# Kernel tuning notes

Measured on AMD Instinct MI355X. Metric: run time of the kernel, lower is better.

Reference implementation:

```python
import jax, jax.numpy as jnp
import numpy as np
import math
from jax import lax

L, E, H, F = 4, 1024, 16, 4096
B, S = 8, 512
VV, VR = 40, 30
DIST_V = 200
PAD_ID = 0


def setup_inputs() -> dict:
    key = jax.random.key(0)
    ks = iter(jax.random.split(key, 32))
    w = lambda *sh: jax.random.normal(next(ks), sh, jnp.float32) * 0.02
    inp = {
        'val_emb': w(VV, E),
        'ring_emb': w(VR, E),
        'dist_emb': w(DIST_V, H),
        'Wqkv': w(L, 3 * E, E), 'bqkv': jnp.zeros((L, 3 * E), jnp.float32),
        'Wo': w(L, E, E), 'bo': jnp.zeros((L, E), jnp.float32),
        'ln1_s': jnp.ones((L, E), jnp.float32), 'ln1_b': jnp.zeros((L, E), jnp.float32),
        'W1': w(L, F, E), 'b1': jnp.zeros((L, F), jnp.float32),
        'W2': w(L, E, F), 'b2': jnp.zeros((L, E), jnp.float32),
        'ln2_s': jnp.ones((L, E), jnp.float32), 'ln2_b': jnp.zeros((L, E), jnp.float32),
        'lnf_s': jnp.ones((E,), jnp.float32), 'lnf_b': jnp.zeros((E,), jnp.float32),
        'gen_W': w(VV * VR, E), 'gen_b': jnp.zeros((VV * VR,), jnp.float32),
    }
    val = jax.random.randint(next(ks), (B, S), 0, VV)
    val = val.at[:, 0].set(1)  # ensure first key is never <pad> (id 0)
    inp['val_sequences'] = val
    inp['ring_sequences'] = jax.random.randint(next(ks), (B, S), 0, VR)
    inp['distance_squares'] = jax.random.randint(next(ks), (B, S, S), 0, DIST_V)
    return inp


def _ln(x, s, b):
    m = x.mean(-1, keepdims=True)
    v = ((x - m) ** 2).mean(-1, keepdims=True)
    return (x - m) / jnp.sqrt(v + 1e-5) * s + b


def _forward(val_emb, ring_emb, dist_emb, Wqkv, bqkv, Wo, bo, ln1_s, ln1_b,
             W1, b1, W2, b2, ln2_s, ln2_b, lnf_s, lnf_b, gen_W, gen_b,
             val_sequences, ring_sequences, distance_squares):
    Bv, Sv = val_sequences.shape
    dh = E // H
    scale = 1.0 / math.sqrt(dh)
    # token embeddings, each scaled by sqrt(emb_size)
    x = (val_emb[val_sequences] + ring_emb[ring_sequences]) * math.sqrt(E)  # [B,S,E]
    # distance bias [B,S,S,H] -> [B,H,S,S], causal fill with -inf, key padding -inf
    bias = jnp.transpose(dist_emb[distance_squares], (0, 3, 1, 2))
    causal = jnp.tril(jnp.ones((Sv, Sv), bool))
    mask = jnp.where(causal[None, None], bias, -jnp.inf)
    pad = (val_sequences == PAD_ID)  # [B,S]
    mask = jnp.where(pad[:, None, None, :], -jnp.inf, mask)

    def step(h, p):
        wqkv, bq, wo, bo_, l1s, l1b, w1, b1_, w2, b2_, l2s, l2b = p
        qkv = h @ wqkv.T + bq  # [B,S,3E]
        q, k, v = jnp.split(qkv, 3, axis=-1)
        q = q.reshape(Bv, Sv, H, dh).transpose(0, 2, 1, 3)
        k = k.reshape(Bv, Sv, H, dh).transpose(0, 2, 1, 3)
        v = v.reshape(Bv, Sv, H, dh).transpose(0, 2, 1, 3)
        scores = jnp.einsum('bhqd,bhkd->bhqk', q, k) * scale + mask
        a = jax.nn.softmax(scores, axis=-1)
        ctx = jnp.einsum('bhqk,bhkd->bhqd', a, v)
        ctx = ctx.transpose(0, 2, 1, 3).reshape(Bv, Sv, E)
        h = _ln(h + ctx @ wo.T + bo_, l1s, l1b)  # post-norm
        ff = jax.nn.gelu(h @ w1.T + b1_, approximate=False) @ w2.T + b2_
        h = _ln(h + ff, l2s, l2b)
        return h, None

    layer_params = (Wqkv, bqkv, Wo, bo, ln1_s, ln1_b, W1, b1, W2, b2, ln2_s, ln2_b)
    x, _ = lax.scan(step, x, layer_params)
    x = _ln(x, lnf_s, lnf_b)
    return x @ gen_W.T + gen_b  # [B,S,VV*VR]


def reference(val_emb, ring_emb, dist_emb, Wqkv, bqkv, Wo, bo, ln1_s, ln1_b,
              W1, b1, W2, b2, ln2_s, ln2_b, lnf_s, lnf_b, gen_W, gen_b,
              val_sequences, ring_sequences, distance_squares):
    return _forward(val_emb, ring_emb, dist_emb, Wqkv, bqkv, Wo, bo, ln1_s, ln1_b,
                    W1, b1, W2, b2, ln2_s, ln2_b, lnf_s, lnf_b, gen_W, gen_b,
                    val_sequences, ring_sequences, distance_squares)
```

## Files before the change

### kernel.cpp

```cpp
#include <hip/hip_runtime.h>
#include <hip/hip_bf16.h>

typedef __attribute__((ext_vector_type(8))) short bf16x8;
typedef __attribute__((ext_vector_type(4))) float f32x4;
typedef unsigned short u16;
typedef __attribute__((ext_vector_type(4))) unsigned short u16x4;

#define L_ 4
#define E_ 1024
#define H_ 16
#define F_ 4096
#define B_ 8
#define S_ 512
#define T_ 4096
#define GEN_N 1200
#define GEN_PAD 1280
#define D8S 528

#define AS1 __attribute__((address_space(1)))
#define AS3 __attribute__((address_space(3)))

static __device__ __forceinline__ u16 f2bf(float f) {
  unsigned u = __float_as_uint(f);
  unsigned r = (u + 0x7fffu + ((u >> 16) & 1u)) >> 16;
  return (u16)r;
}

static __device__ __forceinline__ unsigned cvt_pk_bf16(float lo, float hi) {
  unsigned r;
  asm("v_cvt_pk_bf16_f32 %0, %1, %2" : "=v"(r) : "v"(lo), "v"(hi));
  return r;
}

static __device__ __forceinline__ float fast_gelu(float v) {
  float y = 0.7978845608f * (v + 0.044715f * v * v * v);
  y = fminf(fmaxf(y, -9.f), 9.f);
  float e2 = __expf(2.f * y);
  float th = (e2 - 1.f) / (e2 + 1.f);
  return 0.5f * v * (1.f + th);
}

__global__ __launch_bounds__(256) void cvt_bf16(const float* __restrict__ src,
                                                u16* __restrict__ dst, int n) {
  int i = (blockIdx.x * 256 + threadIdx.x) * 4;
  if (i >= n) return;
  float4 v = *reinterpret_cast<const float4*>(src + i);
  u16x4 o = {f2bf(v.x), f2bf(v.y), f2bf(v.z), f2bf(v.w)};
  *reinterpret_cast<u16x4*>(dst + i) = o;
}

__global__ __launch_bounds__(256) void cvt4_k(const float* __restrict__ s0,
                                              const float* __restrict__ s1,
                                              const float* __restrict__ s2,
                                              const float* __restrict__ s3,
                                              u16* __restrict__ d0, u16* __restrict__ d1,
                                              u16* __restrict__ d2, u16* __restrict__ d3) {
  int q = blockIdx.x * 256 + threadIdx.x;
  const float* s;
  u16* d;
  int i;
  if (q < 786432) { s = s0; d = d0; i = q; }
  else if (q < 786432 + 262144) { s = s1; d = d1; i = q - 786432; }
  else if (q < 786432 + 262144 + 1048576) { s = s2; d = d2; i = q - (786432 + 262144); }
  else { s = s3; d = d3; i = q - (786432 + 262144 + 1048576); }
  i *= 4;
  float4 v = *reinterpret_cast<const float4*>(s + i);
  u16x4 o = {f2bf(v.x), f2bf(v.y), f2bf(v.z), f2bf(v.w)};
  *reinterpret_cast<u16x4*>(d + i) = o;
}

__global__ __launch_bounds__(256) void d8pre_k(const int* __restrict__ dist,
                                               const int* __restrict__ vseq,
                                               unsigned char* __restrict__ d8g) {
  int idx = blockIdx.x * 256 + threadIdx.x;
  int k4 = idx & 127;
  int b = idx >> 16;
  int4 dv = *reinterpret_cast<const int4*>(dist + (size_t)idx * 4);
  int4 vv = *reinterpret_cast<const int4*>(vseq + b * S_ + k4 * 4);
  uchar4 o;
  o.x = (vv.x == 0) ? (unsigned char)200 : (unsigned char)dv.x;
  o.y = (vv.y == 0) ? (unsigned char)200 : (unsigned char)dv.y;
  o.z = (vv.z == 0) ? (unsigned char)200 : (unsigned char)dv.z;
  o.w = (vv.w == 0) ? (unsigned char)200 : (unsigned char)dv.w;
  *reinterpret_cast<uchar4*>(d8g + (size_t)idx * 4) = o;
}

__global__ __launch_bounds__(256) void embed_k(const float* __restrict__ val_emb,
                                               const float* __restrict__ ring_emb,
                                               const int* __restrict__ vseq,
                                               const int* __restrict__ rseq,
                                               float* __restrict__ h, u16* __restrict__ xbf) {
  int tok = blockIdx.x;
  int e = threadIdx.x * 4;
  int v = vseq[tok], r = rseq[tok];
  float4 a = *reinterpret_cast<const float4*>(val_emb + v * E_ + e);
  float4 b = *reinterpret_cast<const float4*>(ring_emb + r * E_ + e);
  float4 o;
  o.x = (a.x + b.x) * 32.f; o.y = (a.y + b.y) * 32.f;
  o.z = (a.z + b.z) * 32.f; o.w = (a.w + b.w) * 32.f;
  *reinterpret_cast<float4*>(h + (size_t)tok * E_ + e) = o;
  u16x4 ob = {f2bf(o.x), f2bf(o.y), f2bf(o.z), f2bf(o.w)};
  *reinterpret_cast<u16x4*>(xbf + (size_t)tok * E_ + e) = ob;
}

__global__ __launch_bounds__(256) void ln_k(const float* hin, const float* add0,
                                            const float* add1, const float* cbias,
                                            const float* g, const float* bta,
                                            float* hout, u16* xout) {
  int tok = blockIdx.x * 4 + (threadIdx.x >> 6);
  int lane = threadIdx.x & 63;
  const float* hp = hin + (size_t)tok * E_;
  float4 v[4];
  #pragma unroll
  for (int p = 0; p < 4; ++p) {
    int e = p * 256 + lane * 4;
    v[p] = *reinterpret_cast<const float4*>(hp + e);
    if (add0) {
      float4 a0 = *reinterpret_cast<const float4*>(add0 + (size_t)tok * E_ + e);
      float4 a1 = *reinterpret_cast<const float4*>(add1 + (size_t)tok * E_ + e);
      float4 cb = *reinterpret_cast<const float4*>(cbias + e);
      v[p].x += a0.x + a1.x + cb.x; v[p].y += a0.y + a1.y + cb.y;
      v[p].z += a0.z + a1.z + cb.z; v[p].w += a0.w + a1.w + cb.w;
    }
  }
  float s = 0.f, q = 0.f;
  #pragma unroll
  for (int p = 0; p < 4; ++p) {
    s += v[p].x + v[p].y + v[p].z + v[p].w;
    q += v[p].x * v[p].x + v[p].y * v[p].y + v[p].z * v[p].z + v[p].w * v[p].w;
  }
  #pragma unroll
  for (int off = 1; off < 64; off <<= 1) {
    s += __shfl_xor(s, off, 64);
    q += __shfl_xor(q, off, 64);
  }
  float mean = s * (1.f / E_);
  float var = q * (1.f / E_) - mean * mean;
  float inv = rsqrtf(var + 1e-5f);
  #pragma unroll
  for (int p = 0; p < 4; ++p) {
    int e = p * 256 + lane * 4;
    float4 gg = *reinterpret_cast<const float4*>(g + e);
    float4 bb = *reinterpret_cast<const float4*>(bta + e);
    float4 o;
    o.x = (v[p].x - mean) * inv * gg.x + bb.x;
    o.y = (v[p].y - mean) * inv * gg.y + bb.y;
    o.z = (v[p].z - mean) * inv * gg.z + bb.z;
    o.w = (v[p].w - mean) * inv * gg.w + bb.w;
    if (hout) *reinterpret_cast<float4*>(hout + (size_t)tok * E_ + e) = o;
    u16x4 ob = {f2bf(o.x), f2bf(o.y), f2bf(o.z), f2bf(o.w)};
    *reinterpret_cast<u16x4*>(xout + (size_t)tok * E_ + e) = ob;
  }
}

template <int EPI>
__global__ __launch_bounds__(256, 2) void gemm_small(const u16* __restrict__ A,
                                                     const u16* __restrict__ W,
                                                     const float* __restrict__ bias,
                                                     void* __restrict__ Cp,
                                                     u16* __restrict__ Vt,
                                                     int M, int N, int K, int tilesN) {
  __shared__ __align__(16) char lds[49152];
  int tid = threadIdx.x;
  int wid = tid >> 6, l = tid & 63;
  int wm = wid >> 1, wn = wid & 1;
  int lr = l & 15, lk = l >> 4;
  int nwg = gridDim.x, bid = blockIdx.x;
  int swz = ((nwg & 7) == 0) ? ((bid & 7) * (nwg >> 3) + (bid >> 3)) : bid;
  int tm = swz / tilesN, tn = swz % tilesN;
  int row0 = tm * 128, col0 = tn * 256;

  int srow = tid >> 2;
  int sch = ((tid & 3) ^ ((srow >> 1) & 3)) * 8;
  const u16* gA = A + (size_t)(row0 + srow) * K + sch;
  const u16* gB = W + (size_t)(col0 + srow) * K + sch;
  int wslot = wid * 1024;

  auto stage = [&](int buf, int kt) {
    size_t ko = (size_t)kt * 32;
    int base = buf * 24576;
    #pragma unroll
    for (int i = 0; i < 2; ++i)
      __builtin_amdgcn_global_load_lds((const AS1 void*)(gA + (size_t)i * 64 * K + ko),
                                       (AS3 void*)(lds + base + i * 4096 + wslot), 16, 0, 0);
    #pragma unroll
    for (int i = 0; i < 4; ++i)
      __builtin_amdgcn_global_load_lds((const AS1 void*)(gB + (size_t)i * 64 * K + ko),
                                       (AS3 void*)(lds + base + 8192 + i * 4096 + wslot), 16, 0, 0);
  };

  int ck = (lk ^ ((lr >> 1) & 3)) * 16;
  f32x4 acc[4][8];
  f32x4 z = {0.f, 0.f, 0.f, 0.f};
  #pragma unroll
  for (int m = 0; m < 4; ++m)
    #pragma unroll
    for (int n = 0; n < 8; ++n) acc[m][n] = z;

  auto compute = [&](int buf) {
    int base = buf * 24576;
    bf16x8 bfr[8];
    #pragma unroll
    for (int n = 0; n < 8; ++n)
      bfr[n] = *reinterpret_cast<const bf16x8*>(lds + base + 8192 + (wn * 128 + n * 16 + lr) * 64 + ck);
    #pragma unroll
    for (int m = 0; m < 4; ++m) {
      bf16x8 af = *reinterpret_cast<const bf16x8*>(lds + base + (wm * 64 + m * 16 + lr) * 64 + ck);
      #pragma unroll
      for (int n = 0; n < 8; ++n)
        acc[m][n] = __builtin_amdgcn_mfma_f32_16x16x32_bf16(af, bfr[n], acc[m][n], 0, 0, 0);
    }
  };

  int nt = K >> 5;
  stage(0, 0);
  int cur = 0;
  for (int t = 0; t < nt; ++t) {
    if (t + 1 < nt) {
      stage(cur ^ 1, t + 1);
      asm volatile("s_waitcnt vmcnt(6)" ::: "memory");
    } else {
      asm volatile("s_waitcnt vmcnt(0)" ::: "memory");
    }
    __builtin_amdgcn_s_barrier();
    asm volatile("" ::: "memory");
    compute(cur);
    asm volatile("" ::: "memory");
    __builtin_amdgcn_s_barrier();
    cur ^= 1;
  }

  #pragma unroll
  for (int n = 0; n < 8; ++n) {
    int col = col0 + wn * 128 + n * 16 + lr;
    float bv = bias[col];
    #pragma unroll
    for (int m = 0; m < 4; ++m) {
      int rbase = row0 + wm * 64 + m * 16 + lk * 4;
      #pragma unroll
      for (int r2 = 0; r2 < 4; ++r2) {
        float v = acc[m][n][r2] + bv;
        if (EPI == 1) v = fast_gelu(v);
        int row = rbase + r2;
        u16 bw = f2bf(v);
        ((u16*)Cp)[(size_t)row * N + col] = bw;
        if (EPI == 0 && Vt != nullptr && col >= 2 * E_) {
          int dg = col - 2 * E_;
          int hh = dg >> 6, dd = dg & 63;
          int bb = row >> 9, ss = row & 511;
          Vt[((size_t)((bb * 16 + hh) * 64 + dd) << 9) + ss] = bw;
        }
      }
    }
  }
}

template <int EPI, int NW, int SPLITK>
__global__ __launch_bounds__(512, 2) void gemm_big(const u16* __restrict__ A,
                                                   const u16* __restrict__ W,
                                                   const float* __restrict__ bias,
                                                   void* __restrict__ Cp,
                                                   int M, int N, int K, int tilesN) {
  constexpr int BN = 64 * NW;
  __shared__ __align__(16) u16 As[2][256 * 64];
  __shared__ __align__(16) u16 Bs[2][BN * 64];
  int tid = threadIdx.x;
  int wid = tid >> 6, ln = tid & 63;
  int wm = wid >> 2, wn = wid & 3;
  int lr = ln & 15, lk = ln >> 4;
  int nwg = gridDim.x;
  int bid = blockIdx.x;
  int swz = ((nwg & 7) == 0) ? ((bid & 7) * (nwg >> 3) + (bid >> 3)) : bid;
  int sp = 0, tile = swz;
  if (SPLITK > 1) { sp = swz & (SPLITK - 1); tile = swz / SPLITK; }
  int tm = tile / tilesN, tn = tile % tilesN;
  int row0 = tm * 256, col0 = tn * BN;
  int Ks = K / SPLITK;
  int kbase = sp * Ks;

  int srow = tid >> 3;
  int schunk = ((tid & 7) ^ (srow & 7)) * 8;
  const u16* gA = A + (size_t)(row0 + srow) * K + kbase + schunk;
  const u16* gB = W + (size_t)(col0 + srow) * K + kbase + schunk;
  size_t ldsBase = (size_t)((wid << 3) * 64) * 2;

  auto stage = [&](int buf, int kt) {
    size_t ko = (size_t)kt * 64;
    #pragma unroll
    for (int i = 0; i < 4; ++i)
      __builtin_amdgcn_global_load_lds(
          (const AS1 void*)(gA + (size_t)i * 64 * K + ko),
          (AS3 void*)((char*)&As[buf][0] + ldsBase + (size_t)i * 64 * 128), 16, 0, 0);
    #pragma unroll
    for (int i = 0; i < NW; ++i)
      __builtin_amdgcn_global_load_lds(
          (const AS1 void*)(gB + (size_t)i * 64 * K + ko),
          (AS3 void*)((char*)&Bs[buf][0] + ldsBase + (size_t)i * 64 * 128), 16, 0, 0);
  };

  f32x4 acc[8][NW];
  f32x4 z = {0.f, 0.f, 0.f, 0.f};
  #pragma unroll
  for (int m = 0; m < 8; ++m)
    #pragma unroll
    for (int n = 0; n < NW; ++n) acc[m][n] = z;

  auto compute = [&](int buf) {
    #pragma unroll
    for (int s = 0; s < 2; ++s) {
      int ch = ((s * 4 + lk) ^ (lr & 7)) * 8;
      bf16x8 bfr[NW];
      #pragma unroll
      for (int n = 0; n < NW; ++n)
        bfr[n] = *reinterpret_cast<const bf16x8*>(&Bs[buf][(wn * (16 * NW) + n * 16 + lr) * 64 + ch]);
      #pragma unroll
      for (int m = 0; m < 8; ++m) {
        bf16x8 af = *reinterpret_cast<const bf16x8*>(&As[buf][(wm * 128 + m * 16 + lr) * 64 + ch]);
        #pragma unroll
        for (int n = 0; n < NW; ++n)
          acc[m][n] = __builtin_amdgcn_mfma_f32_16x16x32_bf16(af, bfr[n], acc[m][n], 0, 0, 0);
      }
    }
  };

  int nt = Ks >> 6;
  stage(0, 0);
  int cur = 0;
  for (int t = 0; t < nt; ++t) {
    if (t + 1 < nt) {
      stage(cur ^ 1, t + 1);
      if constexpr (NW == 2) asm volatile("s_waitcnt vmcnt(6)" ::: "memory");
      else if constexpr (NW == 3) asm volatile("s_waitcnt vmcnt(7)" ::: "memory");
      else asm volatile("s_waitcnt vmcnt(8)" ::: "memory");
    } else {
      asm volatile("s_waitcnt vmcnt(0)" ::: "memory");
    }
    __builtin_amdgcn_s_barrier();
    asm volatile("" ::: "memory");
    compute(cur);
    asm volatile("" ::: "memory");
    __builtin_amdgcn_s_barrier();
    cur ^= 1;
  }

  #pragma unroll
  for (int n = 0; n < NW; ++n) {
    int col = col0 + wn * (16 * NW) + n * 16 + lr;
    if (col >= N) continue;
    float bv = (EPI == 2) ? 0.f : bias[col];
    #pragma unroll
    for (int m = 0; m < 8; ++m) {
      int rbase = row0 + wm * 128 + m * 16 + lk * 4;
      #pragma unroll
      for (int r2 = 0; r2 < 4; ++r2) {
        float v = acc[m][n][r2] + bv;
        int row = rbase + r2;
        if (EPI == 2)
          ((float*)Cp)[(size_t)sp * M * N + (size_t)row * N + col] = v;
        else
          ((float*)Cp)[(size_t)row * N + col] = v;
      }
    }
  }
}

__global__ __launch_bounds__(256, 4) void attn_fused_k(const u16* __restrict__ qkv,
                                                       const unsigned char* __restrict__ d8g,
                                                       const float* __restrict__ dist_emb,
                                                       const u16* __restrict__ Vt,
                                                       u16* __restrict__ ctx) {
  int blk = blockIdx.x;
  int bh = blk & 127;
  int qt = blk >> 7;
  int b = bh >> 4, h = bh & 15;
  int tid = threadIdx.x, wv = tid >> 6, l = tid & 63;
  int lr = l & 15, lk = l >> 4;

  __shared__ float de[208];
  __shared__ __align__(16) unsigned char d8[64 * D8S];

  int ncol = (qt + 1) * 64;
  for (int i = tid; i < 208; i += 256)
    de[i] = (i < 200) ? dist_emb[i * H_ + h] : -1e30f;
  {
    int r = tid >> 2;
    const unsigned char* srow = d8g + ((size_t)(b * S_ + qt * 64 + r) << 9);
    int nc16 = ncol >> 4;
    for (int c = (tid & 3); c < nc16; c += 4) {
      int4 v = *reinterpret_cast<const int4*>(srow + c * 16);
      *reinterpret_cast<int4*>(&d8[r * D8S + c * 16]) = v;
    }
  }
  __syncthreads();

  int q0 = qt * 64 + wv * 16;
  int nv = 4 * qt + wv + 1;
  int qglob = q0 + lr;
  int qloc = wv * 16 + lr;

  bf16x8 aq0 = *reinterpret_cast<const bf16x8*>(
      qkv + (size_t)(b * S_ + q0 + lr) * 3072 + h * 64 + lk * 8);
  bf16x8 aq1 = *reinterpret_cast<const bf16x8*>(
      qkv + (size_t)(b * S_ + q0 + lr) * 3072 + h * 64 + 32 + lk * 8);

  float sm = 0.f;
  f32x4 z = {0.f, 0.f, 0.f, 0.f};
  f32x4 acc_o[4] = {z, z, z, z};

  int sA = lr + ((2 * lk) & 3) * 16;
  int sB = lr + ((2 * lk + 1) & 3) * 16;
  int jsel = (lk >= 2);

  const u16* kBase = qkv + (size_t)(b * S_ + lr) * 3072 + E_ + h * 64 + lk * 8;
  const u16* vBase = Vt + (size_t)(bh * 64 + lr) * S_ + lk * 8;

  int ngroups = (nv + 1) >> 1;
  #pragma unroll 1
  for (int g = 0; g < ngroups; ++g) {
    f32x4 s0 = z, s1 = z;
    {
      const u16* kb = kBase + (size_t)(2 * g) * 16 * 3072;
      bf16x8 bk0 = *reinterpret_cast<const bf16x8*>(kb);
      bf16x8 bk1 = *reinterpret_cast<const bf16x8*>(kb + 32);
      s0 = __builtin_amdgcn_mfma_f32_16x16x32_bf16(bk0, aq0, s0, 0, 0, 0);
      s0 = __builtin_amdgcn_mfma_f32_16x16x32_bf16(bk1, aq1, s0, 0, 0, 0);
    }
    if (2 * g + 1 < nv) {
      const u16* kb = kBase + (size_t)(2 * g + 1) * 16 * 3072;
      bf16x8 bk0 = *reinterpret_cast<const bf16x8*>(kb);
      bf16x8 bk1 = *reinterpret_cast<const bf16x8*>(kb + 32);
      s1 = __builtin_amdgcn_mfma_f32_16x16x32_bf16(bk0, aq0, s1, 0, 0, 0);
      s1 = __builtin_amdgcn_mfma_f32_16x16x32_bf16(bk1, aq1, s1, 0, 0, 0);
    }
    float e0[4], e1[4];
    {
      unsigned dd = *reinterpret_cast<const unsigned*>(&d8[qloc * D8S + (2 * g) * 16 + lk * 4]);
      #pragma unroll
      for (int r2 = 0; r2 < 4; ++r2) {
        int kg = (2 * g) * 16 + lk * 4 + r2;
        float e = 0.f;
        if (kg <= qglob)
          e = __expf(s0[r2] * 0.125f + de[(dd >> (8 * r2)) & 255]);
        e0[r2] = e; sm += e;
      }
    }
    {
      unsigned dd = *reinterpret_cast<const unsigned*>(&d8[qloc * D8S + (2 * g + 1) * 16 + lk * 4]);
      #pragma unroll
      for (int r2 = 0; r2 < 4; ++r2) {
        int kg = (2 * g + 1) * 16 + lk * 4 + r2;
        float e = 0.f;
        if (2 * g + 1 < nv && kg <= qglob)
          e = __expf(s1[r2] * 0.125f + de[(dd >> (8 * r2)) & 255]);
        e1[r2] = e; sm += e;
      }
    }
    unsigned t0p0 = cvt_pk_bf16(e0[0], e0[1]);
    unsigned t0p1 = cvt_pk_bf16(e0[2], e0[3]);
    unsigned t1p0 = cvt_pk_bf16(e1[0], e1[1]);
    unsigned t1p1 = cvt_pk_bf16(e1[2], e1[3]);
    unsigned a00 = __shfl((int)t0p0, sA, 64), a10 = __shfl((int)t1p0, sA, 64);
    unsigned a01 = __shfl((int)t0p1, sA, 64), a11 = __shfl((int)t1p1, sA, 64);
    unsigned b00 = __shfl((int)t0p0, sB, 64), b10 = __shfl((int)t1p0, sB, 64);
    unsigned b01 = __shfl((int)t0p1, sB, 64), b11 = __shfl((int)t1p1, sB, 64);
    unsigned w0 = jsel ? a10 : a00;
    unsigned w1 = jsel ? a11 : a01;
    unsigned w2 = jsel ? b10 : b00;
    unsigned w3 = jsel ? b11 : b01;
    bf16x8 pfrag;
    {
      unsigned pw[4] = {w0, w1, w2, w3};
      pfrag = *reinterpret_cast<bf16x8*>(pw);
    }
    const u16* vb = vBase + g * 32;
    acc_o[0] = __builtin_amdgcn_mfma_f32_16x16x32_bf16(
        *reinterpret_cast<const bf16x8*>(vb), pfrag, acc_o[0], 0, 0, 0);
    acc_o[1] = __builtin_amdgcn_mfma_f32_16x16x32_bf16(
        *reinterpret_cast<const bf16x8*>(vb + 16 * S_), pfrag, acc_o[1], 0, 0, 0);
    acc_o[2] = __builtin_amdgcn_mfma_f32_16x16x32_bf16(
        *reinterpret_cast<const bf16x8*>(vb + 32 * S_), pfrag, acc_o[2], 0, 0, 0);
    acc_o[3] = __builtin_amdgcn_mfma_f32_16x16x32_bf16(
        *reinterpret_cast<const bf16x8*>(vb + 48 * S_), pfrag, acc_o[3], 0, 0, 0);
  }

  sm += __shfl_xor(sm, 16, 64);
  sm += __shfl_xor(sm, 32, 64);
  float il = 1.f / sm;

  #pragma unroll
  for (int n4 = 0; n4 < 4; ++n4) {
    u16x4 o;
    o.x = f2bf(acc_o[n4][0] * il);
    o.y = f2bf(acc_o[n4][1] * il);
    o.z = f2bf(acc_o[n4][2] * il);
    o.w = f2bf(acc_o[n4][3] * il);
    *reinterpret_cast<u16x4*>(ctx + (size_t)(b * S_ + qglob) * E_ + h * 64 + n4 * 16 + lk * 4) = o;
  }
}

extern "C" void kernel_launch(void* const* d_in, const int* in_sizes, int n_in,
                              void* d_out, int out_size, void* d_ws, size_t ws_size,
                              hipStream_t stream) {
  const float* val_emb = (const float*)d_in[0];
  const float* ring_emb = (const float*)d_in[1];
  const float* dist_emb = (const float*)d_in[2];
  const float* Wqkv = (const float*)d_in[3];
  const float* bqkv = (const float*)d_in[4];
  const float* Wo = (const float*)d_in[5];
  const float* bo = (const float*)d_in[6];
  const float* ln1_s = (const float*)d_in[7];
  const float* ln1_b = (const float*)d_in[8];
  const float* W1 = (const float*)d_in[9];
  const float* b1 = (const float*)d_in[10];
  const float* W2 = (const float*)d_in[11];
  const float* b2 = (const float*)d_in[12];
  const float* ln2_s = (const float*)d_in[13];
  const float* ln2_b = (const float*)d_in[14];
  const float* lnf_s = (const float*)d_in[15];
  const float* lnf_b = (const float*)d_in[16];
  const float* gen_W = (const float*)d_in[17];
  const float* gen_b = (const float*)d_in[18];
  const int* vseq = (const int*)d_in[19];
  const int* rseq = (const int*)d_in[20];
  const int* dist = (const int*)d_in[21];

  char* ws = (char*)d_ws;
  size_t off = 0;
  auto alloc = [&](size_t nbytes) {
    char* p = ws + off;
    off += (nbytes + 255) & ~(size_t)255;
    return p;
  };
  u16* gw_bf = (u16*)alloc((size_t)GEN_PAD * E_ * 2);
  u16* wqkv_l = (u16*)alloc((size_t)3 * E_ * E_ * 2);
  u16* wo_l = (u16*)alloc((size_t)E_ * E_ * 2);
  u16* w1_l = (u16*)alloc((size_t)F_ * E_ * 2);
  u16* w2_l = (u16*)alloc((size_t)E_ * F_ * 2);
  float* h = (float*)alloc((size_t)T_ * E_ * 4);
  u16* x_bf = (u16*)alloc((size_t)T_ * E_ * 2);
  u16* qkv_bf = (u16*)alloc((size_t)T_ * 3 * E_ * 2);
  u16* ctx_bf = (u16*)alloc((size_t)T_ * E_ * 2);
  u16* vt_bf = (u16*)alloc((size_t)B_ * H_ * 64 * S_ * 2);
  unsigned char* d8g = (unsigned char*)alloc((size_t)B_ * S_ * S_);
  u16* p_bf = (u16*)alloc((size_t)B_ * H_ * S_ * S_ * 2);
  u16* ff_bf = p_bf;
  float* psum = (float*)(p_bf + (size_t)T_ * F_);
  (void)ws_size; (void)in_sizes; (void)n_in; (void)out_size; (void)rseq;

  cvt_bf16<<<dim3((GEN_N * E_ / 4 + 255) / 256), dim3(256), 0, stream>>>(gen_W, gw_bf,
                                                                         GEN_N * E_);
  d8pre_k<<<dim3(B_ * S_ * S_ / 4 / 256), dim3(256), 0, stream>>>(dist, vseq, d8g);
  embed_k<<<dim3(T_), dim3(256), 0, stream>>>(val_emb, ring_emb, vseq, rseq, h, x_bf);

  for (int l = 0; l < L_; ++l) {
    cvt4_k<<<dim3(12288), dim3(256), 0, stream>>>(
        Wqkv + (size_t)l * 3 * E_ * E_, Wo + (size_t)l * E_ * E_,
        W1 + (size_t)l * F_ * E_, W2 + (size_t)l * E_ * F_,
        wqkv_l, wo_l, w1_l, w2_l);

    gemm_small<0><<<dim3(384), dim3(256), 0, stream>>>(
        x_bf, wqkv_l, bqkv + (size_t)l * 3 * E_, qkv_bf, vt_bf, T_, 3 * E_, E_, 12);
    attn_fused_k<<<dim3(B_ * H_ * 8), dim3(256), 0, stream>>>(qkv_bf, d8g, dist_emb,
                                                              vt_bf, ctx_bf);
    gemm_big<2, 2, 2><<<dim3(256), dim3(512), 0, stream>>>(
        ctx_bf, wo_l, nullptr, psum, T_, E_, E_, 8);
    ln_k<<<dim3(T_ / 4), dim3(256), 0, stream>>>(h, psum, psum + (size_t)T_ * E_,
                                                 bo + (size_t)l * E_,
                                                 ln1_s + (size_t)l * E_, ln1_b + (size_t)l * E_,
                                                 h, x_bf);
    gemm_small<1><<<dim3(512), dim3(256), 0, stream>>>(
        x_bf, w1_l, b1 + (size_t)l * F_, ff_bf, nullptr, T_, F_, E_, 16);
    gemm_big<2, 2, 2><<<dim3(256), dim3(512), 0, stream>>>(
        ff_bf, w2_l, nullptr, psum, T_, E_, F_, 8);
    ln_k<<<dim3(T_ / 4), dim3(256), 0, stream>>>(h, psum, psum + (size_t)T_ * E_,
                                                 b2 + (size_t)l * E_,
                                                 ln2_s + (size_t)l * E_, ln2_b + (size_t)l * E_,
                                                 h, x_bf);
  }
  ln_k<<<dim3(T_ / 4), dim3(256), 0, stream>>>(h, nullptr, nullptr, nullptr, lnf_s, lnf_b,
                                               nullptr, x_bf);
  gemm_big<3, 2, 1><<<dim3(160), dim3(512), 0, stream>>>(
      x_bf, gw_bf, gen_b, (float*)d_out, T_, GEN_N, E_, 10);
}
```

Measured before the change: 1.022 ms.

## Add 256x256 ping-pong GEMM kernel for FFN and split W2 GEMM four ways

Adds a new 512-thread GEMM kernel, gemm8p. It uses 256x256 tiles, a swizzled LDS layout and eight interleaved compute phases with staged loads and priority bumps, and it replaces the W1 and W2 FFN GEMMs. The W2 GEMM now uses split-K of 4 with partials written to two buffers, one of them reusing the qkv buffer. The layernorm kernel takes two extra partial-sum inputs to reduce these. The intent is larger tile reuse and better MFMA/load overlap. The cost is higher register and LDS pressure at occupancy 1, plus extra partial traffic in the LN.

```diff
diff --git a/kernel.cpp b/kernel.cpp
--- a/kernel.cpp
+++ b/kernel.cpp
@@ -104,7 +104,8 @@
 }
 
 __global__ __launch_bounds__(256) void ln_k(const float* hin, const float* add0,
-                                            const float* add1, const float* cbias,
+                                            const float* add1, const float* add2,
+                                            const float* add3, const float* cbias,
                                             const float* g, const float* bta,
                                             float* hout, u16* xout) {
   int tok = blockIdx.x * 4 + (threadIdx.x >> 6);
@@ -121,6 +122,12 @@
       float4 cb = *reinterpret_cast<const float4*>(cbias + e);
       v[p].x += a0.x + a1.x + cb.x; v[p].y += a0.y + a1.y + cb.y;
       v[p].z += a0.z + a1.z + cb.z; v[p].w += a0.w + a1.w + cb.w;
+      if (add2) {
+        float4 a2 = *reinterpret_cast<const float4*>(add2 + (size_t)tok * E_ + e);
+        float4 a3 = *reinterpret_cast<const float4*>(add3 + (size_t)tok * E_ + e);
+        v[p].x += a2.x + a3.x; v[p].y += a2.y + a3.y;
+        v[p].z += a2.z + a3.z; v[p].w += a2.w + a3.w;
+      }
     }
   }
   float s = 0.f, q = 0.f;
@@ -150,6 +157,178 @@
     if (hout) *reinterpret_cast<float4*>(hout + (size_t)tok * E_ + e) = o;
     u16x4 ob = {f2bf(o.x), f2bf(o.y), f2bf(o.z), f2bf(o.w)};
     *reinterpret_cast<u16x4*>(xout + (size_t)tok * E_ + e) = ob;
+  }
+}
+
+template <int EPI, int SPLITK>
+__global__ __launch_bounds__(512, 1) void gemm8p(const u16* __restrict__ A,
+                                                 const u16* __restrict__ W,
+                                                 const float* __restrict__ bias,
+                                                 void* __restrict__ Cp,
+                                                 float* __restrict__ Cp2,
+                                                 int M, int N, int K, int tilesN) {
+  __shared__ __align__(16) u16 As[2][256 * 64];
+  __shared__ __align__(16) u16 Bs[2][256 * 64];
+  int tid = threadIdx.x;
+  int wid = tid >> 6, l = tid & 63;
+  int wm = wid >> 2, wn = wid & 3;
+  int lr = l & 15, lk = l >> 4;
+  int nwg = gridDim.x, bid = blockIdx.x;
+  int swz = ((nwg & 7) == 0) ? ((bid & 7) * (nwg >> 3) + (bid >> 3)) : bid;
+  int sp = 0, tile = swz;
+  if (SPLITK > 1) { sp = swz & (SPLITK - 1); tile = swz / SPLITK; }
+  int tm = tile / tilesN, tn = tile % tilesN;
+  int row0 = tm * 256, col0 = tn * 256;
+  int Ks = K / SPLITK, kbase = sp * Ks;
+
+  int srow = tid >> 3;
+  int schunk = ((tid & 7) ^ (srow & 7)) * 8;
+  const u16* gA = A + (size_t)(row0 + srow) * K + kbase + schunk;
+  const u16* gB = W + (size_t)(col0 + srow) * K + kbase + schunk;
+  size_t ldsBase = (size_t)wid * 1024;
+
+  auto stageHalf = [&](int buf, int kt, int half) {
+    size_t ko = (size_t)kt * 64;
+    if (half == 0) {
+      __builtin_amdgcn_global_load_lds((const AS1 void*)(gA + ko),
+          (AS3 void*)((char*)&As[buf][0] + ldsBase), 16, 0, 0);
+      __builtin_amdgcn_global_load_lds((const AS1 void*)(gA + (size_t)64 * K + ko),
+          (AS3 void*)((char*)&As[buf][0] + 8192 + ldsBase), 16, 0, 0);
+    } else if (half == 1) {
+      __builtin_amdgcn_global_load_lds((const AS1 void*)(gA + (size_t)128 * K + ko),
+          (AS3 void*)((char*)&As[buf][0] + 16384 + ldsBase), 16, 0, 0);
+      __builtin_amdgcn_global_load_lds((const AS1 void*)(gA + (size_t)192 * K + ko),
+          (AS3 void*)((char*)&As[buf][0] + 24576 + ldsBase), 16, 0, 0);
+    } else if (half == 2) {
+      __builtin_amdgcn_global_load_lds((const AS1 void*)(gB + ko),
+          (AS3 void*)((char*)&Bs[buf][0] + ldsBase), 16, 0, 0);
+      __builtin_amdgcn_global_load_lds((const AS1 void*)(gB + (size_t)64 * K + ko),
+          (AS3 void*)((char*)&Bs[buf][0] + 8192 + ldsBase), 16, 0, 0);
+    } else {
+      __builtin_amdgcn_global_load_lds((const AS1 void*)(gB + (size_t)128 * K + ko),
+          (AS3 void*)((char*)&Bs[buf][0] + 16384 + ldsBase), 16, 0, 0);
+      __builtin_amdgcn_global_load_lds((const AS1 void*)(gB + (size_t)192 * K + ko),
+          (AS3 void*)((char*)&Bs[buf][0] + 24576 + ldsBase), 16, 0, 0);
+    }
+  };
+
+  f32x4 acc[8][4];
+  f32x4 z = {0.f, 0.f, 0.f, 0.f};
+  #pragma unroll
+  for (int m = 0; m < 8; ++m)
+    #pragma unroll
+    for (int n = 0; n < 4; ++n) acc[m][n] = z;
+
+  bf16x8 aF[4][2], aS[4][2], bF[2][2], bS[2][2];
+
+  auto ldA4 = [&](bf16x8 (&dst)[4][2], int buf, int mBase) {
+    #pragma unroll
+    for (int m = 0; m < 4; ++m)
+      #pragma unroll
+      for (int s = 0; s < 2; ++s) {
+        int row = wm * 128 + (mBase + m) * 16 + lr;
+        int ch = ((s * 4 + lk) ^ (lr & 7)) * 8;
+        dst[m][s] = *reinterpret_cast<const bf16x8*>(&As[buf][row * 64 + ch]);
+      }
+  };
+  auto ldB2 = [&](bf16x8 (&dst)[2][2], int buf, int nBase) {
+    #pragma unroll
+    for (int n = 0; n < 2; ++n)
+      #pragma unroll
+      for (int s = 0; s < 2; ++s) {
+        int row = wn * 64 + (nBase + n) * 16 + lr;
+        int ch = ((s * 4 + lk) ^ (lr & 7)) * 8;
+        dst[n][s] = *reinterpret_cast<const bf16x8*>(&Bs[buf][row * 64 + ch]);
+      }
+  };
+
+#define PHASE_HEAD() \
+    asm volatile("" ::: "memory"); \
+    __builtin_amdgcn_s_barrier(); \
+    asm volatile("s_waitcnt lgkmcnt(0)" ::: "memory"); \
+    __builtin_amdgcn_s_setprio(1);
+#define PHASE_TAIL() \
+    __builtin_amdgcn_s_setprio(0); \
+    asm volatile("" ::: "memory"); \
+    __builtin_amdgcn_s_barrier(); \
+    asm volatile("" ::: "memory");
+#define MM_Q(AREG, BREG, MB, NB) \
+    _Pragma("unroll") \
+    for (int m = 0; m < 4; ++m) \
+      _Pragma("unroll") \
+      for (int n = 0; n < 2; ++n) \
+        _Pragma("unroll") \
+        for (int s = 0; s < 2; ++s) \
+          acc[(MB) + m][(NB) + n] = __builtin_amdgcn_mfma_f32_16x16x32_bf16( \
+              AREG[m][s], BREG[n][s], acc[(MB) + m][(NB) + n], 0, 0, 0);
+
+  int nt = Ks >> 6;
+  int nIter = nt >> 1;
+  stageHalf(0, 0, 0); stageHalf(0, 0, 1); stageHalf(0, 0, 2); stageHalf(0, 0, 3);
+  stageHalf(1, 1, 0);
+  asm volatile("s_waitcnt vmcnt(2)" ::: "memory");
+  __builtin_amdgcn_s_barrier();
+  asm volatile("" ::: "memory");
+
+  for (int i = 0; i < nIter; ++i) {
+    int a = 2 * i, b = 2 * i + 1;
+    bool notLast = (i < nIter - 1);
+    ldA4(aF, 0, 0); ldB2(bF, 0, 0);
+    stageHalf(1, b, 1);
+    PHASE_HEAD(); MM_Q(aF, bF, 0, 0); PHASE_TAIL();
+    ldB2(bS, 0, 2);
+    stageHalf(1, b, 2);
+    PHASE_HEAD(); MM_Q(aF, bS, 0, 2); PHASE_TAIL();
+    ldA4(aS, 0, 4);
+    stageHalf(1, b, 3);
+    PHASE_HEAD(); MM_Q(aS, bF, 4, 0); PHASE_TAIL();
+    if (notLast) {
+      stageHalf(0, a + 2, 0);
+      asm volatile("s_waitcnt vmcnt(2)" ::: "memory");
+    } else {
+      asm volatile("s_waitcnt vmcnt(0)" ::: "memory");
+    }
+    PHASE_HEAD(); MM_Q(aS, bS, 4, 2); PHASE_TAIL();
+    ldA4(aF, 1, 0); ldB2(bF, 1, 0);
+    if (notLast) stageHalf(0, a + 2, 1);
+    PHASE_HEAD(); MM_Q(aF, bF, 0, 0); PHASE_TAIL();
+    ldB2(bS, 1, 2);
+    if (notLast) stageHalf(0, a + 2, 2);
+    PHASE_HEAD(); MM_Q(aF, bS, 0, 2); PHASE_TAIL();
+    ldA4(aS, 1, 4);
+    if (notLast) stageHalf(0, a + 2, 3);
+    PHASE_HEAD(); MM_Q(aS, bF, 4, 0); PHASE_TAIL();
+    if (notLast) {
+      stageHalf(1, b + 2, 0);
+      asm volatile("s_waitcnt vmcnt(2)" ::: "memory");
+    }
+    PHASE_HEAD(); MM_Q(aS, bS, 4, 2); PHASE_TAIL();
+  }
+#undef PHASE_HEAD
+#undef PHASE_TAIL
+#undef MM_Q
+
+  #pragma unroll
+  for (int n = 0; n < 4; ++n) {
+    int col = col0 + wn * 64 + n * 16 + lr;
+    if (col >= N) continue;
+    float bv = (EPI == 2) ? 0.f : bias[col];
+    #pragma unroll
+    for (int m = 0; m < 8; ++m) {
+      int rbase = row0 + wm * 128 + m * 16 + lk * 4;
+      #pragma unroll
+      for (int r2 = 0; r2 < 4; ++r2) {
+        float v = acc[m][n][r2] + bv;
+        if (EPI == 1) v = fast_gelu(v);
+        int row = rbase + r2;
+        if (EPI == 2) {
+          float* dst = (sp < 2) ? (float*)Cp : Cp2;
+          dst[(size_t)(sp & 1) * M * N + (size_t)row * N + col] = v;
+        } else {
+          ((u16*)Cp)[(size_t)row * N + col] = f2bf(v);
+        }
+      }
+    }
   }
 }
 
@@ -330,7 +509,6 @@
     if (t + 1 < nt) {
       stage(cur ^ 1, t + 1);
       if constexpr (NW == 2) asm volatile("s_waitcnt vmcnt(6)" ::: "memory");
-      else if constexpr (NW == 3) asm volatile("s_waitcnt vmcnt(7)" ::: "memory");
       else asm volatile("s_waitcnt vmcnt(8)" ::: "memory");
     } else {
       asm volatile("s_waitcnt vmcnt(0)" ::: "memory");
@@ -545,6 +723,7 @@
   u16* p_bf = (u16*)alloc((size_t)B_ * H_ * S_ * S_ * 2);
   u16* ff_bf = p_bf;
   float* psum = (float*)(p_bf + (size_t)T_ * F_);
+  float* psum2 = (float*)qkv_bf;
   (void)ws_size; (void)in_sizes; (void)n_in; (void)out_size; (void)rseq;
 
   cvt_bf16<<<dim3((GEN_N * E_ / 4 + 255) / 256), dim3(256), 0, stream>>>(gen_W, gw_bf,
@@ -565,20 +744,21 @@
     gemm_big<2, 2, 2><<<dim3(256), dim3(512), 0, stream>>>(
         ctx_bf, wo_l, nullptr, psum, T_, E_, E_, 8);
     ln_k<<<dim3(T_ / 4), dim3(256), 0, stream>>>(h, psum, psum + (size_t)T_ * E_,
-                                                 bo + (size_t)l * E_,
+                                                 nullptr, nullptr, bo + (size_t)l * E_,
                                                  ln1_s + (size_t)l * E_, ln1_b + (size_t)l * E_,
                                                  h, x_bf);
-    gemm_small<1><<<dim3(512), dim3(256), 0, stream>>>(
+    gemm8p<1, 1><<<dim3(256), dim3(512), 0, stream>>>(
         x_bf, w1_l, b1 + (size_t)l * F_, ff_bf, nullptr, T_, F_, E_, 16);
-    gemm_big<2, 2, 2><<<dim3(256), dim3(512), 0, stream>>>(
-        ff_bf, w2_l, nullptr, psum, T_, E_, F_, 8);
+    gemm8p<2, 4><<<dim3(256), dim3(512), 0, stream>>>(
+        ff_bf, w2_l, nullptr, psum, psum2, T_, E_, F_, 4);
     ln_k<<<dim3(T_ / 4), dim3(256), 0, stream>>>(h, psum, psum + (size_t)T_ * E_,
+                                                 psum2, psum2 + (size_t)T_ * E_,
                                                  b2 + (size_t)l * E_,
                                                  ln2_s + (size_t)l * E_, ln2_b + (size_t)l * E_,
                                                  h, x_bf);
   }
-  ln_k<<<dim3(T_ / 4), dim3(256), 0, stream>>>(h, nullptr, nullptr, nullptr, lnf_s, lnf_b,
-                                               nullptr, x_bf);
+  ln_k<<<dim3(T_ / 4), dim3(256), 0, stream>>>(h, nullptr, nullptr, nullptr, nullptr,
+                                               nullptr, lnf_s, lnf_b, nullptr, x_bf);
   gemm_big<3, 2, 1><<<dim3(160), dim3(512), 0, stream>>>(
       x_bf, gw_bf, gen_b, (float*)d_out, T_, GEN_N, E_, 10);
 }
```

After: 1.028 ms. No clear change (+0.5%).
